# Performance work log

Hardware: AMD Instinct MI355X
Metric: run time of the kernel (lower is better)

Reference implementation:

```python
import jax, jax.numpy as jnp
import numpy as np

BLKQ = 128   # query block size (BLOCK_M)
BLKK = 64    # key block size (BLOCK_N)
TOPK_RATIO = 0.1
EPS = 1e-5


def _block_mean(x, blk):
    # x: (B,H,L,D) -> (B,H,L//blk,D) mean over each block (compress_kernel)
    B, H, L, D = x.shape
    return x.reshape(B, H, L // blk, blk, D).mean(axis=3)


def setup_inputs() -> dict:
    key = jax.random.key(0)
    ks = jax.random.split(key, 5)
    B, L, H, D = 2, 4096, 16, 64
    return {
        "query": jax.random.normal(ks[0], (B, L, H, D), dtype=jnp.float32),
        "key":   jax.random.normal(ks[1], (B, L, H, D), dtype=jnp.float32),
        "value": jax.random.normal(ks[2], (B, L, H, D), dtype=jnp.float32),
        "W": 0.02 * jax.random.normal(ks[3], (D, D), dtype=jnp.float32),
        "b": 0.02 * jax.random.normal(ks[4], (D,), dtype=jnp.float32),
    }


def reference(query, key, value, W, b):
    # inputs (B,L,H,D) -> internal (B,H,L,D)
    q = jnp.transpose(query, (0, 2, 1, 3))
    k = jnp.transpose(key, (0, 2, 1, 3))
    v = jnp.transpose(value, (0, 2, 1, 3))
    B, H, L, D = q.shape
    scale = D ** (-0.5)

    # ---- get_block_map: mean-pooled block scoring + top-k LUT ----
    arg_k = k - k.mean(axis=2, keepdims=True)
    pq = _block_mean(q, BLKQ)        # (B,H,M,D)
    pk = _block_mean(arg_k, BLKK)    # (B,H,KB,D)
    score = jnp.einsum('bhmd,bhkd->bhmk', pq, pk)  # (B,H,M,KB)
    KB = score.shape[-1]
    topk = min(KB, int(TOPK_RATIO * KB))
    _, lut = jax.lax.top_k(score, topk)            # (B,H,M,topk) int32

    # ---- block-sparse attention over gathered K/V blocks ----
    M = L // BLKQ
    kb = k.reshape(B, H, KB, BLKK, D)
    vb = v.reshape(B, H, KB, BLKK, D)
    idx = lut.reshape(B, H, M * topk, 1, 1)
    gk = jnp.take_along_axis(kb, idx, axis=2).reshape(B, H, M, topk * BLKK, D)
    gv = jnp.take_along_axis(vb, idx, axis=2).reshape(B, H, M, topk * BLKK, D)
    qb = q.reshape(B, H, M, BLKQ, D)
    logits = jnp.einsum('bhmqd,bhmnd->bhmqn', qb, gk) * scale
    p = jax.nn.softmax(logits, axis=-1)  # online softmax over union of selected blocks
    o_s = jnp.einsum('bhmqn,bhmnd->bhmqd', p, gv).reshape(B, H, L, D)

    # ---- linear attention branch (feature_map='softmax') ----
    qf = jax.nn.softmax(q, axis=-1)
    kf = jax.nn.softmax(k, axis=-1)
    kv = jnp.einsum('bhld,bhle->bhde', kf, v)
    num = jnp.einsum('bhld,bhde->bhle', qf, kv)
    den = jnp.einsum('bhld,bhd->bhl', qf, kf.sum(axis=2))
    o_l = num / (EPS + den[..., None])
    o_l = jnp.einsum('bhld,ed->bhle', o_l, W) + b  # proj_l

    out = jnp.transpose(o_s + o_l, (0, 2, 1, 3))  # back to (B,L,H,D)
    return out
```

## Files before the change

kernel.cpp:

```cpp
#include <hip/hip_runtime.h>
#include <math.h>
#include <cstdint>
#include <cstddef>

#define B_    2
#define LSEQ  4096
#define H_    16
#define D_    64
#define M_    32
#define KB_   64
#define TOPK  6
#define SCALE 0.125f
#define EPSL  1e-5f
#define SPLIT 32
#define PSTR  65

typedef __attribute__((ext_vector_type(8))) short short8;
typedef __attribute__((ext_vector_type(4))) float f32x4;

#define LGKM_FENCE() __asm__ volatile("s_waitcnt lgkmcnt(0)" ::: "memory")

__device__ __forceinline__ short bf16_rne(float x) {
  unsigned u = __float_as_uint(x);
  return (short)((u + 0x7fffu + ((u >> 16) & 1u)) >> 16);
}
__device__ __forceinline__ unsigned pack2_rne(float a, float b) {
  return ((unsigned)(unsigned short)bf16_rne(a)) | (((unsigned)(unsigned short)bf16_rne(b)) << 16);
}

__global__ __launch_bounds__(256) void lin_stats_kernel(
    const float* __restrict__ kin, const float* __restrict__ vin,
    const float* __restrict__ qin,
    float* __restrict__ kv, float* __restrict__ kfs,
    float* __restrict__ pkw, float* __restrict__ pqw)
{
  int blk   = blockIdx.x;
  int chunk = blk & (SPLIT - 1);
  int bh    = blk / SPLIT;
  int h = bh & (H_ - 1);
  int b = bh >> 4;
  int tid = threadIdx.x;
  int w = tid >> 6, lane = tid & 63, quad = lane >> 4, l15 = lane & 15;

  __shared__ __align__(16) float kraw[64 * 68];
  __shared__ __align__(16) short sA[64 * 64];
  __shared__ __align__(16) short sB[80 * 64];
  __shared__ float pred[512];

  for (int i = tid; i < 1024; i += 256) {
    int row = 64 + (i >> 6);
    sB[row * 64 + (i & 63)] = (row == 64) ? (short)0x3F80 : (short)0;
  }

  {
    int c4 = tid & 15, r0 = tid >> 4;
    float4 s = {0.f, 0.f, 0.f, 0.f};
    for (int i = 0; i < 8; i++) {
      int row = r0 + i * 16;
      float4 x = *(const float4*)(qin + (((size_t)b * LSEQ + chunk * 128 + row) * H_ + h) * D_ + c4 * 4);
      s.x += x.x; s.y += x.y; s.z += x.z; s.w += x.w;
    }
    ((float4*)kraw)[tid] = s;
    __syncthreads();
    if (tid < 16) {
      float4 a = {0.f, 0.f, 0.f, 0.f};
      for (int j = 0; j < 16; j++) {
        float4 x = ((float4*)kraw)[j * 16 + tid];
        a.x += x.x; a.y += x.y; a.z += x.z; a.w += x.w;
      }
      float4 o = {a.x * (1.f/128.f), a.y * (1.f/128.f), a.z * (1.f/128.f), a.w * (1.f/128.f)};
      *(float4*)(pqw + ((size_t)bh * 32 + chunk) * 64 + tid * 4) = o;
    }
  }

  f32x4 acc[5];
#pragma unroll
  for (int nt = 0; nt < 5; nt++) acc[nt] = (f32x4){0.f, 0.f, 0.f, 0.f};

  for (int t2 = 0; t2 < 2; ++t2) {
    int kbs = chunk * 2 + t2;
    int l0  = chunk * 128 + t2 * 64;
    __syncthreads();
#pragma unroll
    for (int i = 0; i < 4; i++) {
      int f = tid + i * 256;
      int row = f >> 4, c4 = f & 15;
      *(float4*)(kraw + row * 68 + c4 * 4) =
        *(const float4*)(kin + (((size_t)b * LSEQ + l0 + row) * H_ + h) * D_ + c4 * 4);
    }
    {
      const float* vp = vin + (((size_t)b * LSEQ + l0 + lane) * H_ + h) * D_ + w * 16;
      float4 a0 = *(const float4*)(vp + 0);
      float4 a1 = *(const float4*)(vp + 4);
      float4 a2 = *(const float4*)(vp + 8);
      float4 a3 = *(const float4*)(vp + 12);
      float f[16] = {a0.x,a0.y,a0.z,a0.w, a1.x,a1.y,a1.z,a1.w,
                     a2.x,a2.y,a2.z,a2.w, a3.x,a3.y,a3.z,a3.w};
#pragma unroll
      for (int j = 0; j < 16; j++) {
        int e = w * 16 + j;
        int col = (((lane >> 3) ^ (e & 7)) << 3) | (lane & 7);
        sB[e * 64 + col] = bf16_rne(f[j]);
      }
    }
    __syncthreads();
    {
      float kp = 0.f;
#pragma unroll
      for (int i = 0; i < 16; i++) kp += kraw[(w * 16 + i) * 68 + lane];
      pred[256 + w * 64 + lane] = kp;
    }
    float kr[16];
    *(float4*)(kr + 0)  = *(const float4*)(kraw + lane * 68 + w * 16 + 0);
    *(float4*)(kr + 4)  = *(const float4*)(kraw + lane * 68 + w * 16 + 4);
    *(float4*)(kr + 8)  = *(const float4*)(kraw + lane * 68 + w * 16 + 8);
    *(float4*)(kr + 12) = *(const float4*)(kraw + lane * 68 + w * 16 + 12);
    float ps = 0.f;
#pragma unroll
    for (int j = 0; j < 16; j++) { kr[j] = __expf(kr[j]); ps += kr[j]; }
    pred[w * 64 + lane] = ps;
    __syncthreads();
    float ssum = pred[lane] + pred[64 + lane] + pred[128 + lane] + pred[192 + lane];
    float scl = 1.f / ssum;
    if (tid < 64) {
      float s = pred[256 + tid] + pred[320 + tid] + pred[384 + tid] + pred[448 + tid];
      pkw[((size_t)bh * 64 + kbs) * 64 + tid] = s * (1.f / 64.f);
    }
#pragma unroll
    for (int j = 0; j < 16; j++) {
      int d = w * 16 + j;
      int col = (((lane >> 3) ^ (d & 7)) << 3) | (lane & 7);
      sA[d * 64 + col] = bf16_rne(kr[j] * scl);
    }
    __syncthreads();
    short8 af[2];
#pragma unroll
    for (int ks = 0; ks < 2; ks++) {
      int row = w * 16 + l15;
      int bi = (ks * 4 + quad) ^ (row & 7);
      af[ks] = *(const short8*)(sA + row * 64 + bi * 8);
    }
#pragma unroll
    for (int nt = 0; nt < 5; nt++) {
      int row = nt * 16 + l15;
#pragma unroll
      for (int ks = 0; ks < 2; ks++) {
        int bi = (ks * 4 + quad) ^ (row & 7);
        short8 bf = *(const short8*)(sB + row * 64 + bi * 8);
        acc[nt] = __builtin_amdgcn_mfma_f32_16x16x32_bf16(af[ks], bf, acc[nt], 0, 0, 0);
      }
    }
  }
  size_t kvb = (size_t)bh * 4096;
  int d0 = w * 16 + quad * 4;
#pragma unroll
  for (int nt = 0; nt < 4; nt++)
#pragma unroll
    for (int r = 0; r < 4; r++)
      atomicAdd(&kv[kvb + (size_t)(d0 + r) * 64 + nt * 16 + l15], acc[nt][r]);
  if (l15 == 0) {
#pragma unroll
    for (int r = 0; r < 4; r++)
      atomicAdd(&kfs[bh * 64 + d0 + r], acc[4][r]);
  }
}

__global__ __launch_bounds__(256) void blockmap_kernel(
    const float* __restrict__ pkw, const float* __restrict__ pqw,
    int* __restrict__ lut)
{
  int bh = blockIdx.x;
  int tid = threadIdx.x;

  __shared__ float pk[64 * PSTR];
  __shared__ float pq[32 * PSTR];
  __shared__ float sc[32 * PSTR];
  __shared__ float km[64];

#pragma unroll
  for (int i = 0; i < 16; i++) {
    int o = tid + i * 256;
    pk[(o >> 6) * PSTR + (o & 63)] = pkw[(size_t)bh * 4096 + o];
  }
#pragma unroll
  for (int i = 0; i < 8; i++) {
    int o = tid + i * 256;
    pq[(o >> 6) * PSTR + (o & 63)] = pqw[(size_t)bh * 2048 + o];
  }
  __syncthreads();
  if (tid < 64) {
    float s = 0.f;
#pragma unroll
    for (int kb = 0; kb < 64; kb++) s += pk[kb * PSTR + tid];
    km[tid] = s * (1.f / 64.f);
  }
  __syncthreads();
#pragma unroll
  for (int i = 0; i < 16; i++) {
    int o = tid + i * 256;
    int kb = o >> 6, d = o & 63;
    pk[kb * PSTR + d] -= km[d];
  }
  __syncthreads();
#pragma unroll
  for (int i = 0; i < 8; i++) {
    int o = tid + i * 256;
    int mb = o >> 6, kb = o & 63;
    float s = 0.f;
#pragma unroll
    for (int d = 0; d < 64; d++) s += pq[mb * PSTR + d] * pk[kb * PSTR + d];
    sc[mb * PSTR + kb] = s;
  }
  __syncthreads();
  if (tid < 32) {
    float* row = sc + tid * PSTR;
    int lb = (bh * M_ + tid) * TOPK;
    for (int s = 0; s < TOPK; s++) {
      float best = -INFINITY; int bi = 0;
      for (int j = 0; j < 64; j++) {
        float v = row[j];
        if (v > best) { best = v; bi = j; }
      }
      lut[lb + s] = bi;
      row[bi] = -INFINITY;
    }
  }
}

__global__ __launch_bounds__(256, 4) void sparse_attn_kernel(
    const float* __restrict__ qin, const float* __restrict__ kin,
    const float* __restrict__ vin, const int* __restrict__ lut,
    const float* __restrict__ kv, const float* __restrict__ kfs,
    const float* __restrict__ Wg, const float* __restrict__ biasg,
    float* __restrict__ out)
{
  int blk = blockIdx.x;
  int x = blk & 7, g = blk >> 3;
  int bh = x * 4 + (g & 3);
  int m  = g >> 2;
  int h = bh & (H_ - 1);
  int b = bh >> 4;
  int t = threadIdx.x;
  int w = t >> 6, lane = t & 63, quad = lane >> 4, l15 = lane & 15;

  __shared__ __align__(16) char smem[37120];
  short* sK  = (short*)smem;
  short* sV  = (short*)(smem + 8192);
  short* sP  = (short*)(smem + 18432);
  short* qfA  = (short*)smem;
  short* skv  = (short*)(smem + 18432);
  short* sW   = (short*)(smem + 28672);
  float* sbias= (float*)(smem + 36864);
  short* wPs = sP + w * 1024;

  for (int i = t; i < 1024; i += 256) {
    int row = 64 + (i >> 6);
    sV[row * 64 + (i & 63)] = (row == 64) ? (short)0x3F80 : (short)0;
  }

  short8 qA[2][2];
#pragma unroll
  for (int mt = 0; mt < 2; mt++) {
    int qrow = m * 128 + w * 32 + mt * 16 + l15;
    const float* qp = qin + (((size_t)b * LSEQ + qrow) * H_ + h) * D_;
#pragma unroll
    for (int ks = 0; ks < 2; ks++) {
      int d0 = ks * 32 + quad * 8;
      float4 a0 = *(const float4*)(qp + d0);
      float4 a1 = *(const float4*)(qp + d0 + 4);
      union { int4 i; short8 s; } u;
      u.i.x = pack2_rne(a0.x * SCALE, a0.y * SCALE);
      u.i.y = pack2_rne(a0.z * SCALE, a0.w * SCALE);
      u.i.z = pack2_rne(a1.x * SCALE, a1.y * SCALE);
      u.i.w = pack2_rne(a1.z * SCALE, a1.w * SCALE);
      qA[mt][ks] = u.s;
    }
  }

  f32x4 O[2][4];
  f32x4 Lacc[2];
#pragma unroll
  for (int mt = 0; mt < 2; mt++) {
#pragma unroll
    for (int dt = 0; dt < 4; dt++) O[mt][dt] = (f32x4){0.f, 0.f, 0.f, 0.f};
    Lacc[mt] = (f32x4){0.f, 0.f, 0.f, 0.f};
  }

  int lbase = (bh * M_ + m) * TOPK;

  for (int s = 0; s < TOPK; s++) {
    int kb = lut[lbase + s];
    __syncthreads();
    {
      int key = t >> 2, c = t & 3;
      const float* kp = kin + (((size_t)b * LSEQ + (size_t)kb * 64 + key) * H_ + h) * D_ + c * 16;
      float4 a0 = *(const float4*)(kp + 0);
      float4 a1 = *(const float4*)(kp + 4);
      float4 a2 = *(const float4*)(kp + 8);
      float4 a3 = *(const float4*)(kp + 12);
      int4 h0, h1;
      h0.x = pack2_rne(a0.x, a0.y);  h0.y = pack2_rne(a0.z, a0.w);
      h0.z = pack2_rne(a1.x, a1.y);  h0.w = pack2_rne(a1.z, a1.w);
      h1.x = pack2_rne(a2.x, a2.y);  h1.y = pack2_rne(a2.z, a2.w);
      h1.z = pack2_rne(a3.x, a3.y);  h1.w = pack2_rne(a3.z, a3.w);
      int base = key * 64;
      int b0 = ((c * 2    ) ^ (key & 7)) << 3;
      int b1 = ((c * 2 + 1) ^ (key & 7)) << 3;
      *(int4*)(sK + base + b0) = h0;
      *(int4*)(sK + base + b1) = h1;
    }
    {
      int vkey = t & 63;
      const float* vp = vin + (((size_t)b * LSEQ + (size_t)kb * 64 + vkey) * H_ + h) * D_ + w * 16;
      float4 a0 = *(const float4*)(vp + 0);
      float4 a1 = *(const float4*)(vp + 4);
      float4 a2 = *(const float4*)(vp + 8);
      float4 a3 = *(const float4*)(vp + 12);
      float f[16] = {a0.x,a0.y,a0.z,a0.w, a1.x,a1.y,a1.z,a1.w,
                     a2.x,a2.y,a2.z,a2.w, a3.x,a3.y,a3.z,a3.w};
#pragma unroll
      for (int j = 0; j < 16; j++) {
        int d = w * 16 + j;
        int col = (((vkey >> 3) ^ (d & 7)) << 3) | (vkey & 7);
        sV[d * 64 + col] = bf16_rne(f[j]);
      }
    }
    __syncthreads();

#pragma unroll
    for (int mt = 0; mt < 2; mt++) {
      f32x4 S[4];
#pragma unroll
      for (int nt = 0; nt < 4; nt++) {
        f32x4 acc = (f32x4){0.f, 0.f, 0.f, 0.f};
        int row = nt * 16 + l15;
#pragma unroll
        for (int ks = 0; ks < 2; ks++) {
          int blk8 = ((ks * 4 + quad) ^ (row & 7)) << 3;
          short8 kh = *(const short8*)(sK + row * 64 + blk8);
          acc = __builtin_amdgcn_mfma_f32_16x16x32_bf16(qA[mt][ks], kh, acc, 0, 0, 0);
        }
        S[nt] = acc;
      }
#pragma unroll
      for (int r = 0; r < 4; r++) {
        int prow = quad * 4 + r;
#pragma unroll
        for (int nt = 0; nt < 4; nt++) {
          int key = nt * 16 + l15;
          int idx = prow * 64 + ((((key >> 3) ^ (prow & 7)) << 3) | (key & 7));
          wPs[idx] = bf16_rne(__expf(S[nt][r]));
        }
      }
      LGKM_FENCE();
      short8 pA[2];
#pragma unroll
      for (int ks = 0; ks < 2; ks++) {
        int blk8 = ((ks * 4 + quad) ^ (l15 & 7)) << 3;
        pA[ks] = *(const short8*)(wPs + l15 * 64 + blk8);
      }
      LGKM_FENCE();
#pragma unroll
      for (int dt = 0; dt < 5; dt++) {
        f32x4 acc = (dt < 4) ? O[mt][dt] : Lacc[mt];
        int row = dt * 16 + l15;
#pragma unroll
        for (int ks = 0; ks < 2; ks++) {
          int blk8 = ((ks * 4 + quad) ^ (row & 7)) << 3;
          short8 vh = *(const short8*)(sV + row * 64 + blk8);
          acc = __builtin_amdgcn_mfma_f32_16x16x32_bf16(pA[ks], vh, acc, 0, 0, 0);
        }
        if (dt < 4) O[mt][dt] = acc; else Lacc[mt] = acc;
      }
    }
  }

#pragma unroll
  for (int mt = 0; mt < 2; mt++)
#pragma unroll
    for (int r = 0; r < 4; r++) {
      float lv = __shfl(Lacc[mt][r], lane & 48);
      float inv = 1.f / lv;
#pragma unroll
      for (int dt = 0; dt < 4; dt++) O[mt][dt][r] *= inv;
    }

  __syncthreads();
  if (t < 128) {
    int qrow = m * 128 + t;
    const float* qp = qin + (((size_t)b * LSEQ + qrow) * H_ + h) * D_;
    float qf[64];
    float ss = 0.f;
#pragma unroll
    for (int i = 0; i < 16; i++) {
      float4 f4 = *(const float4*)(qp + i * 4);
      qf[i*4+0] = __expf(f4.x); qf[i*4+1] = __expf(f4.y);
      qf[i*4+2] = __expf(f4.z); qf[i*4+3] = __expf(f4.w);
      ss += qf[i*4+0] + qf[i*4+1] + qf[i*4+2] + qf[i*4+3];
    }
    float inv = 1.f / ss;
#pragma unroll
    for (int bq = 0; bq < 8; bq++) {
      int4 pk4;
      pk4.x = pack2_rne(qf[bq*8+0] * inv, qf[bq*8+1] * inv);
      pk4.y = pack2_rne(qf[bq*8+2] * inv, qf[bq*8+3] * inv);
      pk4.z = pack2_rne(qf[bq*8+4] * inv, qf[bq*8+5] * inv);
      pk4.w = pack2_rne(qf[bq*8+6] * inv, qf[bq*8+7] * inv);
      *(int4*)(qfA + t * 64 + ((bq ^ (t & 7)) << 3)) = pk4;
    }
  } else {
    int tt = t - 128;
#pragma unroll
    for (int i = 0; i < 32; i++) {
      int idx = tt + i * 128;
      int d = idx >> 6, e = idx & 63;
      int c1 = (((d >> 3) ^ (e & 7)) << 3) | (d & 7);
      skv[e * 64 + c1] = bf16_rne(kv[(size_t)bh * 4096 + idx]);
    }
#pragma unroll
    for (int j = 0; j < 8; j++) {
      int idx2 = tt + j * 128;
      int row = 64 + (idx2 >> 6), col = idx2 & 63;
      skv[row * 64 + col] = (row == 64) ? bf16_rne(kfs[bh * 64 + col]) : (short)0;
    }
#pragma unroll
    for (int i = 0; i < 32; i++) {
      int idx = tt + i * 128;
      int eo = idx >> 6, dd = idx & 63;
      int c2 = (((dd >> 3) ^ (eo & 7)) << 3) | (dd & 7);
      sW[eo * 64 + c2] = bf16_rne(Wg[idx]);
    }
    if (tt < 64) sbias[tt] = biasg[tt];
  }
  __syncthreads();

  short8 af[2][2];
#pragma unroll
  for (int mt = 0; mt < 2; mt++)
#pragma unroll
    for (int ks = 0; ks < 2; ks++) {
      int arow = w * 32 + mt * 16 + l15;
      int blk8 = ((ks * 4 + quad) ^ (arow & 7)) << 3;
      af[mt][ks] = *(const short8*)(qfA + arow * 64 + blk8);
    }
  LGKM_FENCE();
  short* olS = qfA + (w * 32) * 64;

#pragma unroll
  for (int mt = 0; mt < 2; mt++) {
    f32x4 Cn[5];
#pragma unroll
    for (int nt = 0; nt < 5; nt++) {
      f32x4 acc = (f32x4){0.f, 0.f, 0.f, 0.f};
      int row = nt * 16 + l15;
#pragma unroll
      for (int ks = 0; ks < 2; ks++) {
        int blk8 = ((ks * 4 + quad) ^ (row & 7)) << 3;
        short8 bf = *(const short8*)(skv + row * 64 + blk8);
        acc = __builtin_amdgcn_mfma_f32_16x16x32_bf16(af[mt][ks], bf, acc, 0, 0, 0);
      }
      Cn[nt] = acc;
    }
#pragma unroll
    for (int r = 0; r < 4; r++) {
      float dv = __shfl(Cn[4][r], lane & 48);
      float invd = 1.f / (EPSL + dv);
      int prow = quad * 4 + r;
#pragma unroll
      for (int nt = 0; nt < 4; nt++) {
        int e = nt * 16 + l15;
        int idx = prow * 64 + ((((e >> 3) ^ (prow & 7)) << 3) | (e & 7));
        olS[idx] = bf16_rne(Cn[nt][r] * invd);
      }
    }
    LGKM_FENCE();
    short8 oh[2];
#pragma unroll
    for (int ks = 0; ks < 2; ks++) {
      int blk8 = ((ks * 4 + quad) ^ (l15 & 7)) << 3;
      oh[ks] = *(const short8*)(olS + l15 * 64 + blk8);
    }
    LGKM_FENCE();
#pragma unroll
    for (int nt = 0; nt < 4; nt++) {
      int row = nt * 16 + l15;
      f32x4 acc = O[mt][nt];
#pragma unroll
      for (int ks = 0; ks < 2; ks++) {
        int blk8 = ((ks * 4 + quad) ^ (row & 7)) << 3;
        short8 wf = *(const short8*)(sW + row * 64 + blk8);
        acc = __builtin_amdgcn_mfma_f32_16x16x32_bf16(oh[ks], wf, acc, 0, 0, 0);
      }
      O[mt][nt] = acc;
    }
  }

#pragma unroll
  for (int mt = 0; mt < 2; mt++) {
    int qrow0 = m * 128 + w * 32 + mt * 16 + quad * 4;
#pragma unroll
    for (int r = 0; r < 4; r++) {
      float* op = out + (((size_t)b * LSEQ + qrow0 + r) * H_ + h) * D_ + l15;
#pragma unroll
      for (int dt = 0; dt < 4; dt++)
        op[dt * 16] = O[mt][dt][r] + sbias[dt * 16 + l15];
    }
  }
}

extern "C" void kernel_launch(void* const* d_in, const int* in_sizes, int n_in,
                              void* d_out, int out_size, void* d_ws, size_t ws_size,
                              hipStream_t stream)
{
  const float* q    = (const float*)d_in[0];
  const float* k    = (const float*)d_in[1];
  const float* v    = (const float*)d_in[2];
  const float* W    = (const float*)d_in[3];
  const float* bias = (const float*)d_in[4];
  float* out = (float*)d_out;

  float* kv  = (float*)d_ws;
  float* kfs = kv  + (size_t)B_ * H_ * D_ * D_;
  float* pkw = kfs + (size_t)B_ * H_ * D_;
  float* pqw = pkw + (size_t)B_ * H_ * KB_ * D_;
  int*   lut = (int*)(pqw + (size_t)B_ * H_ * M_ * D_);

  size_t zero_bytes = ((size_t)B_ * H_ * D_ * D_ + (size_t)B_ * H_ * D_) * sizeof(float);
  hipMemsetAsync(d_ws, 0, zero_bytes, stream);

  hipLaunchKernelGGL(lin_stats_kernel,  dim3(B_ * H_ * SPLIT), dim3(256), 0, stream,
                     k, v, q, kv, kfs, pkw, pqw);
  hipLaunchKernelGGL(blockmap_kernel,   dim3(B_ * H_),         dim3(256), 0, stream, pkw, pqw, lut);
  hipLaunchKernelGGL(sparse_attn_kernel,dim3(B_ * H_ * M_),    dim3(256), 0, stream,
                     q, k, v, lut, kv, kfs, W, bias, out);
}
```

Baseline: 231.3 us.

## Prefetch next K/V block, fold log2e into Q, and compute query features in registers

The sparse attention loop now loads the LUT up front and prefetches the next selected K/V block into registers while the current block is computed. Folding log2e into the Q scale lets exp2 replace __expf. The softmax feature map for queries is now computed from the register Q fragments, with row sums taken by an MFMA against a ones vector, which removes the shared-memory qfA pass and a global reload of Q. The launch bounds change from 4 to 3 blocks and __syncthreads is replaced by a raw waitcnt plus s_barrier. The register prefetch raises register pressure and lowers occupancy, and recomputing query features from bf16-rounded scaled Q changes numerics slightly.

```diff
diff --git a/kernel.cpp b/kernel.cpp
--- a/kernel.cpp
+++ b/kernel.cpp
@@ -11,6 +11,8 @@
 #define KB_   64
 #define TOPK  6
 #define SCALE 0.125f
+#define LOG2E 1.4426950408889634f
+#define SCL2  (SCALE * LOG2E)
 #define EPSL  1e-5f
 #define SPLIT 32
 #define PSTR  65
@@ -18,7 +20,8 @@
 typedef __attribute__((ext_vector_type(8))) short short8;
 typedef __attribute__((ext_vector_type(4))) float f32x4;
 
-#define LGKM_FENCE() __asm__ volatile("s_waitcnt lgkmcnt(0)" ::: "memory")
+#define LGKM_FENCE()   __asm__ volatile("s_waitcnt lgkmcnt(0)" ::: "memory")
+#define BLOCK_BARRIER() __asm__ volatile("s_waitcnt lgkmcnt(0)\n\ts_barrier" ::: "memory")
 
 __device__ __forceinline__ short bf16_rne(float x) {
   unsigned u = __float_as_uint(x);
@@ -26,6 +29,9 @@
 }
 __device__ __forceinline__ unsigned pack2_rne(float a, float b) {
   return ((unsigned)(unsigned short)bf16_rne(a)) | (((unsigned)(unsigned short)bf16_rne(b)) << 16);
+}
+__device__ __forceinline__ float bf16_to_f32(short s) {
+  return __uint_as_float(((unsigned)(unsigned short)s) << 16);
 }
 
 __global__ __launch_bounds__(256) void lin_stats_kernel(
@@ -61,7 +67,7 @@
       s.x += x.x; s.y += x.y; s.z += x.z; s.w += x.w;
     }
     ((float4*)kraw)[tid] = s;
-    __syncthreads();
+    BLOCK_BARRIER();
     if (tid < 16) {
       float4 a = {0.f, 0.f, 0.f, 0.f};
       for (int j = 0; j < 16; j++) {
@@ -80,7 +86,7 @@
   for (int t2 = 0; t2 < 2; ++t2) {
     int kbs = chunk * 2 + t2;
     int l0  = chunk * 128 + t2 * 64;
-    __syncthreads();
+    BLOCK_BARRIER();
 #pragma unroll
     for (int i = 0; i < 4; i++) {
       int f = tid + i * 256;
@@ -103,7 +109,7 @@
         sB[e * 64 + col] = bf16_rne(f[j]);
       }
     }
-    __syncthreads();
+    BLOCK_BARRIER();
     {
       float kp = 0.f;
 #pragma unroll
@@ -119,7 +125,7 @@
 #pragma unroll
     for (int j = 0; j < 16; j++) { kr[j] = __expf(kr[j]); ps += kr[j]; }
     pred[w * 64 + lane] = ps;
-    __syncthreads();
+    BLOCK_BARRIER();
     float ssum = pred[lane] + pred[64 + lane] + pred[128 + lane] + pred[192 + lane];
     float scl = 1.f / ssum;
     if (tid < 64) {
@@ -132,7 +138,7 @@
       int col = (((lane >> 3) ^ (d & 7)) << 3) | (lane & 7);
       sA[d * 64 + col] = bf16_rne(kr[j] * scl);
     }
-    __syncthreads();
+    BLOCK_BARRIER();
     short8 af[2];
 #pragma unroll
     for (int ks = 0; ks < 2; ks++) {
@@ -227,7 +233,7 @@
   }
 }
 
-__global__ __launch_bounds__(256, 4) void sparse_attn_kernel(
+__global__ __launch_bounds__(256, 3) void sparse_attn_kernel(
     const float* __restrict__ qin, const float* __restrict__ kin,
     const float* __restrict__ vin, const int* __restrict__ lut,
     const float* __restrict__ kv, const float* __restrict__ kfs,
@@ -247,11 +253,11 @@
   short* sK  = (short*)smem;
   short* sV  = (short*)(smem + 8192);
   short* sP  = (short*)(smem + 18432);
-  short* qfA  = (short*)smem;
   short* skv  = (short*)(smem + 18432);
   short* sW   = (short*)(smem + 28672);
   float* sbias= (float*)(smem + 36864);
   short* wPs = sP + w * 1024;
+  short* olS = (short*)smem + w * 1024;
 
   for (int i = t; i < 1024; i += 256) {
     int row = 64 + (i >> 6);
@@ -269,10 +275,10 @@
       float4 a0 = *(const float4*)(qp + d0);
       float4 a1 = *(const float4*)(qp + d0 + 4);
       union { int4 i; short8 s; } u;
-      u.i.x = pack2_rne(a0.x * SCALE, a0.y * SCALE);
-      u.i.y = pack2_rne(a0.z * SCALE, a0.w * SCALE);
-      u.i.z = pack2_rne(a1.x * SCALE, a1.y * SCALE);
-      u.i.w = pack2_rne(a1.z * SCALE, a1.w * SCALE);
+      u.i.x = pack2_rne(a0.x * SCL2, a0.y * SCL2);
+      u.i.y = pack2_rne(a0.z * SCL2, a0.w * SCL2);
+      u.i.z = pack2_rne(a1.x * SCL2, a1.y * SCL2);
+      u.i.w = pack2_rne(a1.z * SCL2, a1.w * SCL2);
       qA[mt][ks] = u.s;
     }
   }
@@ -287,37 +293,42 @@
   }
 
   int lbase = (bh * M_ + m) * TOPK;
+  int kbs_[TOPK];
+#pragma unroll
+  for (int i = 0; i < TOPK; i++) kbs_[i] = lut[lbase + i];
+
+  float4 pk0, pk1, pk2, pk3;
+  float4 pv0, pv1, pv2, pv3;
+  const int kkey = t >> 2, kc = t & 3;
+  const int vkey = t & 63;
+
+  {
+    int kb = kbs_[0];
+    const float* kp = kin + (((size_t)b * LSEQ + (size_t)kb * 64 + kkey) * H_ + h) * D_ + kc * 16;
+    pk0 = *(const float4*)(kp + 0);  pk1 = *(const float4*)(kp + 4);
+    pk2 = *(const float4*)(kp + 8);  pk3 = *(const float4*)(kp + 12);
+    const float* vp = vin + (((size_t)b * LSEQ + (size_t)kb * 64 + vkey) * H_ + h) * D_ + w * 16;
+    pv0 = *(const float4*)(vp + 0);  pv1 = *(const float4*)(vp + 4);
+    pv2 = *(const float4*)(vp + 8);  pv3 = *(const float4*)(vp + 12);
+  }
 
   for (int s = 0; s < TOPK; s++) {
-    int kb = lut[lbase + s];
-    __syncthreads();
+    BLOCK_BARRIER();
     {
-      int key = t >> 2, c = t & 3;
-      const float* kp = kin + (((size_t)b * LSEQ + (size_t)kb * 64 + key) * H_ + h) * D_ + c * 16;
-      float4 a0 = *(const float4*)(kp + 0);
-      float4 a1 = *(const float4*)(kp + 4);
-      float4 a2 = *(const float4*)(kp + 8);
-      float4 a3 = *(const float4*)(kp + 12);
       int4 h0, h1;
-      h0.x = pack2_rne(a0.x, a0.y);  h0.y = pack2_rne(a0.z, a0.w);
-      h0.z = pack2_rne(a1.x, a1.y);  h0.w = pack2_rne(a1.z, a1.w);
-      h1.x = pack2_rne(a2.x, a2.y);  h1.y = pack2_rne(a2.z, a2.w);
-      h1.z = pack2_rne(a3.x, a3.y);  h1.w = pack2_rne(a3.z, a3.w);
-      int base = key * 64;
-      int b0 = ((c * 2    ) ^ (key & 7)) << 3;
-      int b1 = ((c * 2 + 1) ^ (key & 7)) << 3;
+      h0.x = pack2_rne(pk0.x, pk0.y);  h0.y = pack2_rne(pk0.z, pk0.w);
+      h0.z = pack2_rne(pk1.x, pk1.y);  h0.w = pack2_rne(pk1.z, pk1.w);
+      h1.x = pack2_rne(pk2.x, pk2.y);  h1.y = pack2_rne(pk2.z, pk2.w);
+      h1.z = pack2_rne(pk3.x, pk3.y);  h1.w = pack2_rne(pk3.z, pk3.w);
+      int base = kkey * 64;
+      int b0 = ((kc * 2    ) ^ (kkey & 7)) << 3;
+      int b1 = ((kc * 2 + 1) ^ (kkey & 7)) << 3;
       *(int4*)(sK + base + b0) = h0;
       *(int4*)(sK + base + b1) = h1;
     }
     {
-      int vkey = t & 63;
-      const float* vp = vin + (((size_t)b * LSEQ + (size_t)kb * 64 + vkey) * H_ + h) * D_ + w * 16;
-      float4 a0 = *(const float4*)(vp + 0);
-      float4 a1 = *(const float4*)(vp + 4);
-      float4 a2 = *(const float4*)(vp + 8);
-      float4 a3 = *(const float4*)(vp + 12);
-      float f[16] = {a0.x,a0.y,a0.z,a0.w, a1.x,a1.y,a1.z,a1.w,
-                     a2.x,a2.y,a2.z,a2.w, a3.x,a3.y,a3.z,a3.w};
+      float f[16] = {pv0.x,pv0.y,pv0.z,pv0.w, pv1.x,pv1.y,pv1.z,pv1.w,
+                     pv2.x,pv2.y,pv2.z,pv2.w, pv3.x,pv3.y,pv3.z,pv3.w};
 #pragma unroll
       for (int j = 0; j < 16; j++) {
         int d = w * 16 + j;
@@ -325,7 +336,16 @@
         sV[d * 64 + col] = bf16_rne(f[j]);
       }
     }
-    __syncthreads();
+    BLOCK_BARRIER();
+    if (s + 1 < TOPK) {
+      int kb = kbs_[s + 1];
+      const float* kp = kin + (((size_t)b * LSEQ + (size_t)kb * 64 + kkey) * H_ + h) * D_ + kc * 16;
+      pk0 = *(const float4*)(kp + 0);  pk1 = *(const float4*)(kp + 4);
+      pk2 = *(const float4*)(kp + 8);  pk3 = *(const float4*)(kp + 12);
+      const float* vp = vin + (((size_t)b * LSEQ + (size_t)kb * 64 + vkey) * H_ + h) * D_ + w * 16;
+      pv0 = *(const float4*)(vp + 0);  pv1 = *(const float4*)(vp + 4);
+      pv2 = *(const float4*)(vp + 8);  pv3 = *(const float4*)(vp + 12);
+    }
 
 #pragma unroll
     for (int mt = 0; mt < 2; mt++) {
@@ -349,7 +369,7 @@
         for (int nt = 0; nt < 4; nt++) {
           int key = nt * 16 + l15;
           int idx = prow * 64 + ((((key >> 3) ^ (prow & 7)) << 3) | (key & 7));
-          wPs[idx] = bf16_rne(__expf(S[nt][r]));
+          wPs[idx] = bf16_rne(__builtin_amdgcn_exp2f(S[nt][r]));
         }
       }
       LGKM_FENCE();
@@ -385,69 +405,68 @@
       for (int dt = 0; dt < 4; dt++) O[mt][dt][r] *= inv;
     }
 
-  __syncthreads();
-  if (t < 128) {
-    int qrow = m * 128 + t;
-    const float* qp = qin + (((size_t)b * LSEQ + qrow) * H_ + h) * D_;
-    float qf[64];
-    float ss = 0.f;
-#pragma unroll
-    for (int i = 0; i < 16; i++) {
-      float4 f4 = *(const float4*)(qp + i * 4);
-      qf[i*4+0] = __expf(f4.x); qf[i*4+1] = __expf(f4.y);
-      qf[i*4+2] = __expf(f4.z); qf[i*4+3] = __expf(f4.w);
-      ss += qf[i*4+0] + qf[i*4+1] + qf[i*4+2] + qf[i*4+3];
-    }
-    float inv = 1.f / ss;
-#pragma unroll
-    for (int bq = 0; bq < 8; bq++) {
-      int4 pk4;
-      pk4.x = pack2_rne(qf[bq*8+0] * inv, qf[bq*8+1] * inv);
-      pk4.y = pack2_rne(qf[bq*8+2] * inv, qf[bq*8+3] * inv);
-      pk4.z = pack2_rne(qf[bq*8+4] * inv, qf[bq*8+5] * inv);
-      pk4.w = pack2_rne(qf[bq*8+6] * inv, qf[bq*8+7] * inv);
-      *(int4*)(qfA + t * 64 + ((bq ^ (t & 7)) << 3)) = pk4;
-    }
-  } else {
-    int tt = t - 128;
-#pragma unroll
-    for (int i = 0; i < 32; i++) {
-      int idx = tt + i * 128;
-      int d = idx >> 6, e = idx & 63;
-      int c1 = (((d >> 3) ^ (e & 7)) << 3) | (d & 7);
-      skv[e * 64 + c1] = bf16_rne(kv[(size_t)bh * 4096 + idx]);
-    }
-#pragma unroll
-    for (int j = 0; j < 8; j++) {
-      int idx2 = tt + j * 128;
-      int row = 64 + (idx2 >> 6), col = idx2 & 63;
-      skv[row * 64 + col] = (row == 64) ? bf16_rne(kfs[bh * 64 + col]) : (short)0;
-    }
-#pragma unroll
-    for (int i = 0; i < 32; i++) {
-      int idx = tt + i * 128;
-      int eo = idx >> 6, dd = idx & 63;
-      int c2 = (((dd >> 3) ^ (eo & 7)) << 3) | (dd & 7);
-      sW[eo * 64 + c2] = bf16_rne(Wg[idx]);
-    }
-    if (tt < 64) sbias[tt] = biasg[tt];
-  }
-  __syncthreads();
-
-  short8 af[2][2];
-#pragma unroll
-  for (int mt = 0; mt < 2; mt++)
+  BLOCK_BARRIER();
+#pragma unroll
+  for (int i = 0; i < 16; i++) {
+    int idx = t + i * 256;
+    int d = idx >> 6, e = idx & 63;
+    int c1 = (((d >> 3) ^ (e & 7)) << 3) | (d & 7);
+    skv[e * 64 + c1] = bf16_rne(kv[(size_t)bh * 4096 + idx]);
+    int eo = idx >> 6, dd = idx & 63;
+    int c2 = (((dd >> 3) ^ (eo & 7)) << 3) | (dd & 7);
+    sW[eo * 64 + c2] = bf16_rne(Wg[idx]);
+  }
+#pragma unroll
+  for (int j = 0; j < 4; j++) {
+    int idx2 = t + j * 256;
+    int row = 64 + (idx2 >> 6), col = idx2 & 63;
+    skv[row * 64 + col] = (row == 64) ? bf16_rne(kfs[bh * 64 + col]) : (short)0;
+  }
+  if (t < 64) sbias[t] = biasg[t];
+  BLOCK_BARRIER();
+
+  const short8 onesB = {(short)0x3F80,(short)0x3F80,(short)0x3F80,(short)0x3F80,
+                        (short)0x3F80,(short)0x3F80,(short)0x3F80,(short)0x3F80};
+
+#pragma unroll
+  for (int mt = 0; mt < 2; mt++) {
+    float eq[2][8];
+    short8 eqs[2];
 #pragma unroll
     for (int ks = 0; ks < 2; ks++) {
-      int arow = w * 32 + mt * 16 + l15;
-      int blk8 = ((ks * 4 + quad) ^ (arow & 7)) << 3;
-      af[mt][ks] = *(const short8*)(qfA + arow * 64 + blk8);
-    }
-  LGKM_FENCE();
-  short* olS = qfA + (w * 32) * 64;
-
-#pragma unroll
-  for (int mt = 0; mt < 2; mt++) {
+      union { short8 s; short a[8]; } uu; uu.s = qA[mt][ks];
+      union { int4 i; short8 s; } pp;
+      unsigned pw[4];
+#pragma unroll
+      for (int j = 0; j < 8; j++)
+        eq[ks][j] = __builtin_amdgcn_exp2f(8.f * bf16_to_f32(uu.a[j]));
+#pragma unroll
+      for (int j2 = 0; j2 < 4; j2++)
+        pw[j2] = pack2_rne(eq[ks][j2 * 2], eq[ks][j2 * 2 + 1]);
+      pp.i.x = (int)pw[0]; pp.i.y = (int)pw[1]; pp.i.z = (int)pw[2]; pp.i.w = (int)pw[3];
+      eqs[ks] = pp.s;
+    }
+    f32x4 ssv = (f32x4){0.f, 0.f, 0.f, 0.f};
+    ssv = __builtin_amdgcn_mfma_f32_16x16x32_bf16(eqs[0], onesB, ssv, 0, 0, 0);
+    ssv = __builtin_amdgcn_mfma_f32_16x16x32_bf16(eqs[1], onesB, ssv, 0, 0, 0);
+    int srcl = (l15 >> 2) << 4;
+    float s0 = __shfl(ssv[0], srcl);
+    float s1 = __shfl(ssv[1], srcl);
+    float s2 = __shfl(ssv[2], srcl);
+    float s3 = __shfl(ssv[3], srcl);
+    int rr = l15 & 3;
+    float ssrow = (rr == 0) ? s0 : (rr == 1) ? s1 : (rr == 2) ? s2 : s3;
+    float qinv = 1.f / ssrow;
+    short8 qf[2];
+#pragma unroll
+    for (int ks = 0; ks < 2; ks++) {
+      union { int4 i; short8 s; } pp;
+      pp.i.x = (int)pack2_rne(eq[ks][0] * qinv, eq[ks][1] * qinv);
+      pp.i.y = (int)pack2_rne(eq[ks][2] * qinv, eq[ks][3] * qinv);
+      pp.i.z = (int)pack2_rne(eq[ks][4] * qinv, eq[ks][5] * qinv);
+      pp.i.w = (int)pack2_rne(eq[ks][6] * qinv, eq[ks][7] * qinv);
+      qf[ks] = pp.s;
+    }
     f32x4 Cn[5];
 #pragma unroll
     for (int nt = 0; nt < 5; nt++) {
@@ -457,7 +476,7 @@
       for (int ks = 0; ks < 2; ks++) {
         int blk8 = ((ks * 4 + quad) ^ (row & 7)) << 3;
         short8 bf = *(const short8*)(skv + row * 64 + blk8);
-        acc = __builtin_amdgcn_mfma_f32_16x16x32_bf16(af[mt][ks], bf, acc, 0, 0, 0);
+        acc = __builtin_amdgcn_mfma_f32_16x16x32_bf16(qf[ks], bf, acc, 0, 0, 0);
       }
       Cn[nt] = acc;
     }
```

Measured after the change: 213.8 us. 1.08x faster.
